# Performance work log

Measured on AMD Instinct MI355X. Metric: run time of the kernel, lower is better.

The kernel has to match this reference:

```python
import jax, jax.numpy as jnp
import numpy as np

# Module config (matches init_kwargs): SamplesLoss('sinkhorn', debias=False)
BLUR = 0.05
SCALING = 0.8
DIAMETER = 2.0
P = 2


def _eps_schedule():
    # geomloss annealing: eps from diameter**p down to blur**p, factor scaling**p
    eps_final = BLUR ** P
    eps = DIAMETER ** P
    lst = []
    while eps > eps_final:
        lst.append(eps)
        eps = eps * (SCALING ** P)
    lst.append(eps_final)
    return lst


def setup_inputs() -> dict:
    key = jax.random.key(0)
    k1, k2, k3, k4 = jax.random.split(key, 4)
    B, N, M, D = 8, 2048, 2048, 2
    a = jax.random.uniform(k1, (B, N), dtype=jnp.float32)
    a = a / a.sum(-1, keepdims=True)  # probability weights
    b = jax.random.uniform(k2, (B, M), dtype=jnp.float32)
    b = b / b.sum(-1, keepdims=True)
    x = jax.random.uniform(k3, (B, N, D), dtype=jnp.float32)
    y = jax.random.uniform(k4, (B, M, D), dtype=jnp.float32)
    return {"a": a, "x": x, "b": b, "y": y}


def _softmin(eps, C, h):
    # -eps * LSE_j( h_j - C_ij / eps ), stabilized log-domain reduction
    return -eps * jax.nn.logsumexp(h[:, None, :] - C / eps, axis=2)


def reference(a, x, b, y):
    # p=2 cost: C(x,y) = ||x-y||^2 / 2  -> [B, N, M]
    C_xy = 0.5 * jnp.sum((x[:, :, None, :] - y[:, None, :, :]) ** 2, axis=-1)
    C_yx = jnp.swapaxes(C_xy, 1, 2)
    log_a = jnp.log(a)
    log_b = jnp.log(b)

    eps_list = _eps_schedule()
    eps0 = eps_list[0]
    # initialization at the largest temperature
    f = _softmin(eps0, C_xy, log_b)  # [B, N]
    g = _softmin(eps0, C_yx, log_a)  # [B, M]

    # annealed symmetric Sinkhorn iterations (averaged / damped updates)
    for eps in eps_list:
        ft = _softmin(eps, C_xy, log_b + g / eps)
        gt = _softmin(eps, C_yx, log_a + f / eps)
        f = 0.5 * (f + ft)
        g = 0.5 * (g + gt)

    # geomloss detaches the loop potentials; gradients flow only through the
    # last extrapolation step at the final blur temperature.
    f = jax.lax.stop_gradient(f)
    g = jax.lax.stop_gradient(g)
    eps_f = eps_list[-1]
    f_fin = _softmin(eps_f, C_xy, log_b + g / eps_f)
    g_fin = _softmin(eps_f, C_yx, log_a + f / eps_f)

    batch_loss = jnp.sum(a * f_fin, axis=-1) + jnp.sum(b * g_fin, axis=-1)  # [B]
    # border=None -> Samples_Loss returns mean over the batch
    return batch_loss.mean()
```

## Files before the change

### kernel.cpp

```cpp
#include <hip/hip_runtime.h>
#include <cmath>

#define NB 8
#define NPTS 2048
#define NE (NB * NPTS)
#define THREADS 512
#define RPW 4

typedef float v2f __attribute__((ext_vector_type(2)));

#if defined(__has_builtin)
#if __has_builtin(__builtin_amdgcn_exp2f)
#define FAST_EXP2(x) __builtin_amdgcn_exp2f(x)
#else
#define FAST_EXP2(x) exp2f(x)
#endif
#if __has_builtin(__builtin_amdgcn_logf)
#define FAST_LOG2(x) __builtin_amdgcn_logf(x)
#else
#define FAST_LOG2(x) log2f(x)
#endif
#else
#define FAST_EXP2(x) exp2f(x)
#define FAST_LOG2(x) log2f(x)
#endif

template<int CTRL>
__device__ __forceinline__ float dpp_f(float v) {
    return __int_as_float(__builtin_amdgcn_update_dpp(
        __float_as_int(v), __float_as_int(v), CTRL, 0xF, 0xF, false));
}
__device__ __forceinline__ float wred_max(float v) {
    v = fmaxf(v, dpp_f<0xB1>(v));
    v = fmaxf(v, dpp_f<0x4E>(v));
    v = fmaxf(v, dpp_f<0x141>(v));
    v = fmaxf(v, dpp_f<0x140>(v));
    v = fmaxf(v, dpp_f<0x142>(v));
    v = fmaxf(v, dpp_f<0x143>(v));
    return v;
}
__device__ __forceinline__ float wred_sum(float v) {
    v += dpp_f<0xB1>(v);
    v += dpp_f<0x4E>(v);
    v += dpp_f<0x141>(v);
    v += dpp_f<0x140>(v);
    v += dpp_f<0x142>(v);
    v += dpp_f<0x143>(v);
    return v;
}

__global__ __launch_bounds__(THREADS, 8) void sinkhorn_phase(
    const float* __restrict__ x, const float* __restrict__ y,
    const float* __restrict__ loga, const float* __restrict__ logb,
    const float* __restrict__ f_prev, const float* __restrict__ g_prev,
    float* __restrict__ f_next, float* __restrict__ g_next,
    float* __restrict__ Ls,
    float eps, float inv_eps, float c_old, float c_new,
    float mscale, int initPhase)
{
    __shared__ float4 xy4[NPTS / 2];
    __shared__ float2 hc2[NPTS / 2];

    const int blk = blockIdx.x;
    const int side = blk >> 9;
    const int rblk = blk & 511;
    const int batch = rblk >> 6;
    const int rowTile = rblk & 63;

    const float* rowPts; const float* colPts; const float* hlog;
    const float* hpot; const float* ownPrev; float* outPot;
    if (side == 0) { rowPts=x; colPts=y; hlog=logb; hpot=g_prev; ownPrev=f_prev; outPot=f_next; }
    else           { rowPts=y; colPts=x; hlog=loga; hpot=f_prev; ownPrev=g_prev; outPot=g_next; }

    const float LOG2E = 1.4426950408889634f;
    const float LN2 = 0.69314718055994531f;

    const float4* cp4 = ((const float4*)colPts) + (size_t)batch * (NPTS / 2);
    xy4[threadIdx.x]       = cp4[threadIdx.x];
    xy4[threadIdx.x + 512] = cp4[threadIdx.x + 512];

    {
        const float2* cp2 = (const float2*)(colPts + (size_t)batch * NPTS * 2);
        const float* hl = hlog + (size_t)batch * NPTS;
        const float* pp = hpot + (size_t)batch * NPTS;
        float* hcs = (float*)hc2;
        #pragma unroll
        for (int k = 0; k < NPTS / THREADS; k++) {
            int j = threadIdx.x + k * THREADS;
            float2 p = cp2[j];
            float hp = initPhase ? 0.0f : pp[j] * inv_eps;
            hcs[j] = (hl[j] + hp - 0.5f * inv_eps * fmaf(p.x, p.x, p.y * p.y)) * LOG2E;
        }
    }
    __syncthreads();

    const int lane = threadIdx.x & 63;
    const int wv = threadIdx.x >> 6;
    const int row0 = rowTile * 32 + wv * RPW;
    const int gidx0 = batch * NPTS + row0;
    const float2* rp2 = (const float2*)(rowPts + (size_t)batch * NPTS * 2) + row0;
    const float* Lp = Ls + side * NE + gidx0;

    const float sc = inv_eps * LOG2E;
    v2f rxp[2], ryp[2], mestp[2], sp[2];
    #pragma unroll
    for (int p = 0; p < 2; p++) {
        float2 p0 = rp2[2 * p];
        float2 p1 = rp2[2 * p + 1];
        rxp[p] = (v2f){p0.x * sc, p1.x * sc};
        ryp[p] = (v2f){p0.y * sc, p1.y * sc};
        float m0 = initPhase ? 0.0f : Lp[2 * p] * mscale;
        float m1 = initPhase ? 0.0f : Lp[2 * p + 1] * mscale;
        mestp[p] = (v2f){m0, m1};
        sp[p] = (v2f){0.0f, 0.0f};
    }

    #pragma unroll 4
    for (int it = 0; it < NPTS / 128; it++) {
        float4 v = xy4[(it << 6) + lane];
        float2 h = hc2[(it << 6) + lane];
        #pragma unroll
        for (int p = 0; p < 2; p++) {
            v2f h0 = (v2f){h.x, h.x} - mestp[p];
            v2f h1 = (v2f){h.y, h.y} - mestp[p];
            v2f t0 = __builtin_elementwise_fma(rxp[p], (v2f){v.x, v.x},
                        __builtin_elementwise_fma(ryp[p], (v2f){v.y, v.y}, h0));
            v2f t1 = __builtin_elementwise_fma(rxp[p], (v2f){v.z, v.z},
                        __builtin_elementwise_fma(ryp[p], (v2f){v.w, v.w}, h1));
            sp[p] += (v2f){FAST_EXP2(t0.x), FAST_EXP2(t0.y)};
            sp[p] += (v2f){FAST_EXP2(t1.x), FAST_EXP2(t1.y)};
        }
    }
    float s[RPW];
    s[0] = wred_sum(sp[0].x); s[1] = wred_sum(sp[0].y);
    s[2] = wred_sum(sp[1].x); s[3] = wred_sum(sp[1].y);

    int bad = 0;
    if (lane == 63) {
        #pragma unroll
        for (int r = 0; r < RPW; r++)
            bad |= !(s[r] > 1e-30f && s[r] < 1e34f);
    }
    float mesc[RPW] = { mestp[0].x, mestp[0].y, mestp[1].x, mestp[1].y };

    if (__any(bad)) {
        v2f mm[2];
        mm[0] = (v2f){-3.4e38f, -3.4e38f};
        mm[1] = (v2f){-3.4e38f, -3.4e38f};
        #pragma unroll 4
        for (int it = 0; it < NPTS / 128; it++) {
            float4 v = xy4[(it << 6) + lane];
            float2 h = hc2[(it << 6) + lane];
            #pragma unroll
            for (int p = 0; p < 2; p++) {
                v2f h0 = (v2f){h.x, h.x} - mestp[p];
                v2f h1 = (v2f){h.y, h.y} - mestp[p];
                v2f t0 = __builtin_elementwise_fma(rxp[p], (v2f){v.x, v.x},
                            __builtin_elementwise_fma(ryp[p], (v2f){v.y, v.y}, h0));
                v2f t1 = __builtin_elementwise_fma(rxp[p], (v2f){v.z, v.z},
                            __builtin_elementwise_fma(ryp[p], (v2f){v.w, v.w}, h1));
                mm[p] = __builtin_elementwise_max(mm[p],
                            __builtin_elementwise_max(t0, t1));
            }
        }
        float mmsc[RPW] = { mm[0].x, mm[0].y, mm[1].x, mm[1].y };
        #pragma unroll
        for (int r = 0; r < RPW; r++) {
            mmsc[r] = wred_max(mmsc[r]);
            mmsc[r] = __shfl(mmsc[r], 63);
        }
        v2f mmb[2] = { (v2f){mmsc[0], mmsc[1]}, (v2f){mmsc[2], mmsc[3]} };
        sp[0] = (v2f){0.0f, 0.0f};
        sp[1] = (v2f){0.0f, 0.0f};
        #pragma unroll 4
        for (int it = 0; it < NPTS / 128; it++) {
            float4 v = xy4[(it << 6) + lane];
            float2 h = hc2[(it << 6) + lane];
            #pragma unroll
            for (int p = 0; p < 2; p++) {
                v2f h0 = (v2f){h.x, h.x} - mestp[p] - mmb[p];
                v2f h1 = (v2f){h.y, h.y} - mestp[p] - mmb[p];
                v2f t0 = __builtin_elementwise_fma(rxp[p], (v2f){v.x, v.x},
                            __builtin_elementwise_fma(ryp[p], (v2f){v.y, v.y}, h0));
                v2f t1 = __builtin_elementwise_fma(rxp[p], (v2f){v.z, v.z},
                            __builtin_elementwise_fma(ryp[p], (v2f){v.w, v.w}, h1));
                sp[p] += (v2f){FAST_EXP2(t0.x), FAST_EXP2(t0.y)};
                sp[p] += (v2f){FAST_EXP2(t1.x), FAST_EXP2(t1.y)};
            }
        }
        s[0] = wred_sum(sp[0].x); s[1] = wred_sum(sp[0].y);
        s[2] = wred_sum(sp[1].x); s[3] = wred_sum(sp[1].y);
        #pragma unroll
        for (int r = 0; r < RPW; r++) mesc[r] += mmsc[r];
    }

    if (lane == 63) {
        #pragma unroll
        for (int r = 0; r < RPW; r++) {
            float2 p = rp2[r];
            float hr = -0.5f * sc * fmaf(p.x, p.x, p.y * p.y);
            float L = mesc[r] + FAST_LOG2(s[r]);
            float sm = -eps * LN2 * (hr + L);
            outPot[gidx0 + r] = c_old * ownPrev[gidx0 + r] + c_new * sm;
            Ls[side * NE + gidx0 + r] = L;
        }
    }
}

__global__ void log_precompute(const float* __restrict__ a, const float* __restrict__ b,
                               float* __restrict__ loga, float* __restrict__ logb, int n)
{
    int i = blockIdx.x * blockDim.x + threadIdx.x;
    if (i < n) {
        loga[i] = logf(a[i]);
        logb[i] = logf(b[i]);
    }
}

__global__ __launch_bounds__(1024) void loss_reduce(
    const float* __restrict__ a, const float* __restrict__ bw,
    const float* __restrict__ f, const float* __restrict__ g,
    float* __restrict__ out)
{
    const float4* a4 = (const float4*)a;
    const float4* b4 = (const float4*)bw;
    const float4* f4 = (const float4*)f;
    const float4* g4 = (const float4*)g;
    float acc = 0.0f;
    for (int i = threadIdx.x; i < NE / 4; i += 1024) {
        float4 av = a4[i], fv = f4[i], bv = b4[i], gv = g4[i];
        acc += av.x * fv.x + av.y * fv.y + av.z * fv.z + av.w * fv.w;
        acc += bv.x * gv.x + bv.y * gv.y + bv.z * gv.z + bv.w * gv.w;
    }
    acc += __shfl_xor(acc, 32);
    acc += __shfl_xor(acc, 16);
    acc += __shfl_xor(acc, 8);
    acc += __shfl_xor(acc, 4);
    acc += __shfl_xor(acc, 2);
    acc += __shfl_xor(acc, 1);
    __shared__ float wsum[16];
    int wid = threadIdx.x >> 6;
    if ((threadIdx.x & 63) == 0) wsum[wid] = acc;
    __syncthreads();
    if (threadIdx.x < 16) {
        float v = wsum[threadIdx.x];
        v += __shfl_xor(v, 8, 16);
        v += __shfl_xor(v, 4, 16);
        v += __shfl_xor(v, 2, 16);
        v += __shfl_xor(v, 1, 16);
        if (threadIdx.x == 0) out[0] = v * (1.0f / NB);
    }
}

extern "C" void kernel_launch(void* const* d_in, const int* in_sizes, int n_in,
                              void* d_out, int out_size, void* d_ws, size_t ws_size,
                              hipStream_t stream)
{
    const float* a = (const float*)d_in[0];
    const float* x = (const float*)d_in[1];
    const float* b = (const float*)d_in[2];
    const float* y = (const float*)d_in[3];
    float* out = (float*)d_out;

    float* ws = (float*)d_ws;
    float* loga = ws + 0 * NE;
    float* logb = ws + 1 * NE;
    float* fA   = ws + 2 * NE;
    float* gA   = ws + 3 * NE;
    float* fB   = ws + 4 * NE;
    float* gB   = ws + 5 * NE;
    float* Ls   = ws + 6 * NE;

    double eps_list[32];
    int ne = 0;
    const double eps_final = 0.05 * 0.05;
    double eps = 2.0 * 2.0;
    while (eps > eps_final) { eps_list[ne++] = eps; eps *= 0.64; }
    eps_list[ne++] = eps_final;

    log_precompute<<<(NE + 255) / 256, 256, 0, stream>>>(a, b, loga, logb, NE);

    const float* fp = fA; const float* gp = gA;
    float* fn = fB; float* gn = gB;

    auto phase = [&](double e, double e_prev, float c_old, float c_new, int init) {
        sinkhorn_phase<<<1024, THREADS, 0, stream>>>(
            x, y, loga, logb, fp, gp, fn, gn, Ls,
            (float)e, (float)(1.0 / e), c_old, c_new,
            (float)(e_prev / e), init);
    };
    auto swapbuf = [&]() {
        const float* tf = fp; const float* tg = gp;
        fp = fn; gp = gn;
        fn = (float*)tf; gn = (float*)tg;
    };

    phase(eps_list[0], eps_list[0], 0.0f, 1.0f, 1);
    swapbuf();
    double e_prev = eps_list[0];
    for (int k = 0; k < ne; k++) {
        phase(eps_list[k], e_prev, 0.5f, 0.5f, 0);
        e_prev = eps_list[k];
        swapbuf();
    }
    phase(eps_list[ne - 1], e_prev, 0.0f, 1.0f, 0);

    loss_reduce<<<1, 1024, 0, stream>>>(a, b, fn, gn, out);
}
```

Baseline: 299.6 us.

## Double rows per wave, fuse log weights and loss partials into Sinkhorn phase

```diff
diff --git a/kernel.cpp b/kernel.cpp
--- a/kernel.cpp
+++ b/kernel.cpp
@@ -5,7 +5,8 @@
 #define NPTS 2048
 #define NE (NB * NPTS)
 #define THREADS 512
-#define RPW 4
+#define NPAIR 4
+#define RPW (2 * NPAIR)
 
 typedef float v2f __attribute__((ext_vector_type(2)));
 
@@ -49,28 +50,30 @@
     return v;
 }
 
-__global__ __launch_bounds__(THREADS, 8) void sinkhorn_phase(
+__global__ __launch_bounds__(THREADS, 4) void sinkhorn_phase(
     const float* __restrict__ x, const float* __restrict__ y,
-    const float* __restrict__ loga, const float* __restrict__ logb,
+    const float* __restrict__ a, const float* __restrict__ b,
     const float* __restrict__ f_prev, const float* __restrict__ g_prev,
     float* __restrict__ f_next, float* __restrict__ g_next,
     float* __restrict__ Ls,
+    float* __restrict__ partials,
     float eps, float inv_eps, float c_old, float c_new,
-    float mscale, int initPhase)
+    float mscale, int initPhase, int finalPhase)
 {
     __shared__ float4 xy4[NPTS / 2];
     __shared__ float2 hc2[NPTS / 2];
+    __shared__ float pw[8];
 
     const int blk = blockIdx.x;
-    const int side = blk >> 9;
-    const int rblk = blk & 511;
-    const int batch = rblk >> 6;
-    const int rowTile = rblk & 63;
-
-    const float* rowPts; const float* colPts; const float* hlog;
+    const int side = blk >> 8;
+    const int rblk = blk & 255;
+    const int batch = rblk >> 5;
+    const int rowTile = rblk & 31;
+
+    const float* rowPts; const float* colPts; const float* wcol; const float* wrow;
     const float* hpot; const float* ownPrev; float* outPot;
-    if (side == 0) { rowPts=x; colPts=y; hlog=logb; hpot=g_prev; ownPrev=f_prev; outPot=f_next; }
-    else           { rowPts=y; colPts=x; hlog=loga; hpot=f_prev; ownPrev=g_prev; outPot=g_next; }
+    if (side == 0) { rowPts=x; colPts=y; wcol=b; wrow=a; hpot=g_prev; ownPrev=f_prev; outPot=f_next; }
+    else           { rowPts=y; colPts=x; wcol=a; wrow=b; hpot=f_prev; ownPrev=g_prev; outPot=g_next; }
 
     const float LOG2E = 1.4426950408889634f;
     const float LN2 = 0.69314718055994531f;
@@ -81,7 +84,7 @@
 
     {
         const float2* cp2 = (const float2*)(colPts + (size_t)batch * NPTS * 2);
-        const float* hl = hlog + (size_t)batch * NPTS;
+        const float* wl = wcol + (size_t)batch * NPTS;
         const float* pp = hpot + (size_t)batch * NPTS;
         float* hcs = (float*)hc2;
         #pragma unroll
@@ -89,29 +92,30 @@
             int j = threadIdx.x + k * THREADS;
             float2 p = cp2[j];
             float hp = initPhase ? 0.0f : pp[j] * inv_eps;
-            hcs[j] = (hl[j] + hp - 0.5f * inv_eps * fmaf(p.x, p.x, p.y * p.y)) * LOG2E;
+            hcs[j] = FAST_LOG2(wl[j]) +
+                     (hp - 0.5f * inv_eps * fmaf(p.x, p.x, p.y * p.y)) * LOG2E;
         }
     }
     __syncthreads();
 
     const int lane = threadIdx.x & 63;
     const int wv = threadIdx.x >> 6;
-    const int row0 = rowTile * 32 + wv * RPW;
+    const int row0 = rowTile * 64 + wv * RPW;
     const int gidx0 = batch * NPTS + row0;
     const float2* rp2 = (const float2*)(rowPts + (size_t)batch * NPTS * 2) + row0;
     const float* Lp = Ls + side * NE + gidx0;
 
     const float sc = inv_eps * LOG2E;
-    v2f rxp[2], ryp[2], mestp[2], sp[2];
+    v2f rxp[NPAIR], ryp[NPAIR], nmest[NPAIR], sp[NPAIR];
     #pragma unroll
-    for (int p = 0; p < 2; p++) {
+    for (int p = 0; p < NPAIR; p++) {
         float2 p0 = rp2[2 * p];
         float2 p1 = rp2[2 * p + 1];
         rxp[p] = (v2f){p0.x * sc, p1.x * sc};
         ryp[p] = (v2f){p0.y * sc, p1.y * sc};
         float m0 = initPhase ? 0.0f : Lp[2 * p] * mscale;
         float m1 = initPhase ? 0.0f : Lp[2 * p + 1] * mscale;
-        mestp[p] = (v2f){m0, m1};
+        nmest[p] = (v2f){-m0, -m1};
         sp[p] = (v2f){0.0f, 0.0f};
     }
 
@@ -120,9 +124,9 @@
         float4 v = xy4[(it << 6) + lane];
         float2 h = hc2[(it << 6) + lane];
         #pragma unroll
-        for (int p = 0; p < 2; p++) {
-            v2f h0 = (v2f){h.x, h.x} - mestp[p];
-            v2f h1 = (v2f){h.y, h.y} - mestp[p];
+        for (int p = 0; p < NPAIR; p++) {
+            v2f h0 = (v2f){h.x, h.x} + nmest[p];
+            v2f h1 = (v2f){h.y, h.y} + nmest[p];
             v2f t0 = __builtin_elementwise_fma(rxp[p], (v2f){v.x, v.x},
                         __builtin_elementwise_fma(ryp[p], (v2f){v.y, v.y}, h0));
             v2f t1 = __builtin_elementwise_fma(rxp[p], (v2f){v.z, v.z},
@@ -132,8 +136,11 @@
         }
     }
     float s[RPW];
-    s[0] = wred_sum(sp[0].x); s[1] = wred_sum(sp[0].y);
-    s[2] = wred_sum(sp[1].x); s[3] = wred_sum(sp[1].y);
+    #pragma unroll
+    for (int p = 0; p < NPAIR; p++) {
+        s[2 * p]     = wred_sum(sp[p].x);
+        s[2 * p + 1] = wred_sum(sp[p].y);
+    }
 
     int bad = 0;
     if (lane == 63) {
@@ -141,20 +148,24 @@
         for (int r = 0; r < RPW; r++)
             bad |= !(s[r] > 1e-30f && s[r] < 1e34f);
     }
-    float mesc[RPW] = { mestp[0].x, mestp[0].y, mestp[1].x, mestp[1].y };
+    float mesc[RPW];
+    #pragma unroll
+    for (int p = 0; p < NPAIR; p++) {
+        mesc[2 * p] = -nmest[p].x; mesc[2 * p + 1] = -nmest[p].y;
+    }
 
     if (__any(bad)) {
-        v2f mm[2];
-        mm[0] = (v2f){-3.4e38f, -3.4e38f};
-        mm[1] = (v2f){-3.4e38f, -3.4e38f};
+        v2f mm[NPAIR];
+        #pragma unroll
+        for (int p = 0; p < NPAIR; p++) mm[p] = (v2f){-3.4e38f, -3.4e38f};
         #pragma unroll 4
         for (int it = 0; it < NPTS / 128; it++) {
             float4 v = xy4[(it << 6) + lane];
             float2 h = hc2[(it << 6) + lane];
             #pragma unroll
-            for (int p = 0; p < 2; p++) {
-                v2f h0 = (v2f){h.x, h.x} - mestp[p];
-                v2f h1 = (v2f){h.y, h.y} - mestp[p];
+            for (int p = 0; p < NPAIR; p++) {
+                v2f h0 = (v2f){h.x, h.x} + nmest[p];
+                v2f h1 = (v2f){h.y, h.y} + nmest[p];
                 v2f t0 = __builtin_elementwise_fma(rxp[p], (v2f){v.x, v.x},
                             __builtin_elementwise_fma(ryp[p], (v2f){v.y, v.y}, h0));
                 v2f t1 = __builtin_elementwise_fma(rxp[p], (v2f){v.z, v.z},
@@ -163,23 +174,30 @@
                             __builtin_elementwise_max(t0, t1));
             }
         }
-        float mmsc[RPW] = { mm[0].x, mm[0].y, mm[1].x, mm[1].y };
+        float mmsc[RPW];
+        #pragma unroll
+        for (int p = 0; p < NPAIR; p++) {
+            mmsc[2 * p] = mm[p].x; mmsc[2 * p + 1] = mm[p].y;
+        }
         #pragma unroll
         for (int r = 0; r < RPW; r++) {
             mmsc[r] = wred_max(mmsc[r]);
             mmsc[r] = __shfl(mmsc[r], 63);
         }
-        v2f mmb[2] = { (v2f){mmsc[0], mmsc[1]}, (v2f){mmsc[2], mmsc[3]} };
-        sp[0] = (v2f){0.0f, 0.0f};
-        sp[1] = (v2f){0.0f, 0.0f};
+        v2f mmb[NPAIR];
+        #pragma unroll
+        for (int p = 0; p < NPAIR; p++) {
+            mmb[p] = (v2f){mmsc[2 * p], mmsc[2 * p + 1]};
+            sp[p] = (v2f){0.0f, 0.0f};
+        }
         #pragma unroll 4
         for (int it = 0; it < NPTS / 128; it++) {
             float4 v = xy4[(it << 6) + lane];
             float2 h = hc2[(it << 6) + lane];
             #pragma unroll
-            for (int p = 0; p < 2; p++) {
-                v2f h0 = (v2f){h.x, h.x} - mestp[p] - mmb[p];
-                v2f h1 = (v2f){h.y, h.y} - mestp[p] - mmb[p];
+            for (int p = 0; p < NPAIR; p++) {
+                v2f h0 = (v2f){h.x, h.x} + nmest[p] - mmb[p];
+                v2f h1 = (v2f){h.y, h.y} + nmest[p] - mmb[p];
                 v2f t0 = __builtin_elementwise_fma(rxp[p], (v2f){v.x, v.x},
                             __builtin_elementwise_fma(ryp[p], (v2f){v.y, v.y}, h0));
                 v2f t1 = __builtin_elementwise_fma(rxp[p], (v2f){v.z, v.z},
@@ -188,13 +206,17 @@
                 sp[p] += (v2f){FAST_EXP2(t1.x), FAST_EXP2(t1.y)};
             }
         }
-        s[0] = wred_sum(sp[0].x); s[1] = wred_sum(sp[0].y);
-        s[2] = wred_sum(sp[1].x); s[3] = wred_sum(sp[1].y);
-        #pragma unroll
-        for (int r = 0; r < RPW; r++) mesc[r] += mmsc[r];
+        #pragma unroll
+        for (int p = 0; p < NPAIR; p++) {
+            s[2 * p]     = wred_sum(sp[p].x);
+            s[2 * p + 1] = wred_sum(sp[p].y);
+            mesc[2 * p] += mmb[p].x;
+            mesc[2 * p + 1] += mmb[p].y;
+        }
     }
 
     if (lane == 63) {
+        float part = 0.0f;
         #pragma unroll
         for (int r = 0; r < RPW; r++) {
             float2 p = rp2[r];
@@ -203,52 +225,39 @@
             float sm = -eps * LN2 * (hr + L);
             outPot[gidx0 + r] = c_old * ownPrev[gidx0 + r] + c_new * sm;
             Ls[side * NE + gidx0 + r] = L;
-        }
-    }
-}
-
-__global__ void log_precompute(const float* __restrict__ a, const float* __restrict__ b,
-                               float* __restrict__ loga, float* __restrict__ logb, int n)
+            if (finalPhase) part += wrow[gidx0 + r] * sm;
+        }
+        if (finalPhase) pw[wv] = part;
+    }
+    if (finalPhase) {
+        __syncthreads();
+        if (threadIdx.x == 0) {
+            float t = 0.0f;
+            #pragma unroll
+            for (int i = 0; i < 8; i++) t += pw[i];
+            partials[blk] = t;
+        }
+    }
+}
+
+__global__ __launch_bounds__(512) void final_reduce(
+    const float* __restrict__ partials, float* __restrict__ out)
 {
-    int i = blockIdx.x * blockDim.x + threadIdx.x;
-    if (i < n) {
-        loga[i] = logf(a[i]);
-        logb[i] = logf(b[i]);
-    }
-}
-
-__global__ __launch_bounds__(1024) void loss_reduce(
-    const float* __restrict__ a, const float* __restrict__ bw,
-    const float* __restrict__ f, const float* __restrict__ g,
-    float* __restrict__ out)
-{
-    const float4* a4 = (const float4*)a;
-    const float4* b4 = (const float4*)bw;
-    const float4* f4 = (const float4*)f;
-    const float4* g4 = (const float4*)g;
-    float acc = 0.0f;
-    for (int i = threadIdx.x; i < NE / 4; i += 1024) {
-        float4 av = a4[i], fv = f4[i], bv = b4[i], gv = g4[i];
-        acc += av.x * fv.x + av.y * fv.y + av.z * fv.z + av.w * fv.w;
-        acc += bv.x * gv.x + bv.y * gv.y + bv.z * gv.z + bv.w * gv.w;
-    }
-    acc += __shfl_xor(acc, 32);
-    acc += __shfl_xor(acc, 16);
-    acc += __shfl_xor(acc, 8);
-    acc += __shfl_xor(acc, 4);
-    acc += __shfl_xor(acc, 2);
-    acc += __shfl_xor(acc, 1);
-    __shared__ float wsum[16];
-    int wid = threadIdx.x >> 6;
-    if ((threadIdx.x & 63) == 0) wsum[wid] = acc;
+    float v = partials[threadIdx.x];
+    v += __shfl_xor(v, 32);
+    v += __shfl_xor(v, 16);
+    v += __shfl_xor(v, 8);
+    v += __shfl_xor(v, 4);
+    v += __shfl_xor(v, 2);
+    v += __shfl_xor(v, 1);
+    __shared__ float ws8[8];
+    if ((threadIdx.x & 63) == 0) ws8[threadIdx.x >> 6] = v;
     __syncthreads();
-    if (threadIdx.x < 16) {
-        float v = wsum[threadIdx.x];
-        v += __shfl_xor(v, 8, 16);
-        v += __shfl_xor(v, 4, 16);
-        v += __shfl_xor(v, 2, 16);
-        v += __shfl_xor(v, 1, 16);
-        if (threadIdx.x == 0) out[0] = v * (1.0f / NB);
+    if (threadIdx.x == 0) {
+        float t = 0.0f;
+        #pragma unroll
+        for (int i = 0; i < 8; i++) t += ws8[i];
+        out[0] = t * (1.0f / NB);
     }
 }
 
@@ -263,13 +272,12 @@
     float* out = (float*)d_out;
 
     float* ws = (float*)d_ws;
-    float* loga = ws + 0 * NE;
-    float* logb = ws + 1 * NE;
-    float* fA   = ws + 2 * NE;
-    float* gA   = ws + 3 * NE;
-    float* fB   = ws + 4 * NE;
-    float* gB   = ws + 5 * NE;
-    float* Ls   = ws + 6 * NE;
+    float* fA   = ws + 0 * NE;
+    float* gA   = ws + 1 * NE;
+    float* fB   = ws + 2 * NE;
+    float* gB   = ws + 3 * NE;
+    float* Ls   = ws + 4 * NE;
+    float* partials = ws + 6 * NE;
 
     double eps_list[32];
     int ne = 0;
@@ -278,16 +286,15 @@
     while (eps > eps_final) { eps_list[ne++] = eps; eps *= 0.64; }
     eps_list[ne++] = eps_final;
 
-    log_precompute<<<(NE + 255) / 256, 256, 0, stream>>>(a, b, loga, logb, NE);
-
     const float* fp = fA; const float* gp = gA;
     float* fn = fB; float* gn = gB;
 
-    auto phase = [&](double e, double e_prev, float c_old, float c_new, int init) {
-        sinkhorn_phase<<<1024, THREADS, 0, stream>>>(
-            x, y, loga, logb, fp, gp, fn, gn, Ls,
+    auto phase = [&](double e, double e_prev, float c_old, float c_new,
+                     int init, int fin) {
+        sinkhorn_phase<<<512, THREADS, 0, stream>>>(
+            x, y, a, b, fp, gp, fn, gn, Ls, partials,
             (float)e, (float)(1.0 / e), c_old, c_new,
-            (float)(e_prev / e), init);
+            (float)(e_prev / e), init, fin);
     };
     auto swapbuf = [&]() {
         const float* tf = fp; const float* tg = gp;
@@ -295,15 +302,15 @@
         fn = (float*)tf; gn = (float*)tg;
     };
 
-    phase(eps_list[0], eps_list[0], 0.0f, 1.0f, 1);
+    phase(eps_list[0], eps_list[0], 0.0f, 1.0f, 1, 0);
     swapbuf();
     double e_prev = eps_list[0];
     for (int k = 0; k < ne; k++) {
-        phase(eps_list[k], e_prev, 0.5f, 0.5f, 0);
+        phase(eps_list[k], e_prev, 0.5f, 0.5f, 0, 0);
         e_prev = eps_list[k];
         swapbuf();
     }
-    phase(eps_list[ne - 1], e_prev, 0.0f, 1.0f, 0);
-
-    loss_reduce<<<1, 1024, 0, stream>>>(a, b, fn, gn, out);
-}
+    phase(eps_list[ne - 1], e_prev, 0.0f, 1.0f, 0, 1);
+
+    final_reduce<<<1, 512, 0, stream>>>(partials, out);
+}
```

After: 311.2 us. 1.04x slower.
